# Performance work log

Measured on AMD Instinct MI355X. Metric: run time of the kernel, lower is better.

The kernel has to match this reference:

```python
import jax, jax.numpy as jnp
import numpy as np

EPS = 1e-8
TAU = 1.0


def _spatial_adjacency(segments, n_seg):
    # segments: (B, H, W) int. Counts 4-neighbour pixel adjacencies between segments;
    # diagonal counts pixels per segment (self loops kept).
    B, H, W = segments.shape
    b = jnp.arange(B)[:, None]
    adj = jnp.zeros((B, n_seg, n_seg), jnp.float32)
    flat = segments.reshape(B, -1)
    adj = adj.at[b, flat, flat].add(1.0)  # self loops = segment sizes
    s1 = segments[:, :, :-1].reshape(B, -1)
    s2 = segments[:, :, 1:].reshape(B, -1)
    adj = adj.at[b, s1, s2].add(1.0).at[b, s2, s1].add(1.0)
    v1 = segments[:, :-1, :].reshape(B, -1)
    v2 = segments[:, 1:, :].reshape(B, -1)
    adj = adj.at[b, v1, v2].add(1.0).at[b, v2, v1].add(1.0)
    return adj


def _proximity_adjacency(segments, n_seg):
    adj = _spatial_adjacency(segments, n_seg)
    # zero connections of node 0 except its diagonal
    adj = adj.at[:, 1:, 0].set(0.0).at[:, 0, 1:].set(0.0)
    size_node = jnp.diagonal(adj, axis1=-2, axis2=-1)
    new_diag = adj.sum(axis=2) - size_node + 1.0
    idx = jnp.arange(n_seg)
    adj = adj.at[:, idx, idx].set(new_diag)
    # normalize_adjacency(binarize=True, normalize=False)
    return (adj > 0).astype(jnp.float32)


def setup_inputs() -> dict:
    key = jax.random.key(0)
    k1, k2, k3 = jax.random.split(key, 3)
    B, N, D, R = 8, 2048, 384, 64
    H = W = 256
    x = jax.random.normal(k1, (B, N, D), jnp.float32)
    segments = jax.random.randint(k2, (B, H, W), 0, N, jnp.int64)
    prototypes = jax.random.normal(k3, (1, R, D), jnp.float32)
    return {"x": x, "segments": segments, "prototypes": prototypes}


def reference(x, segments, prototypes):
    B, N, D = x.shape
    prox_adj = _proximity_adjacency(segments, N)  # (B, N, N) binary

    # node-presence mask (B, N)
    b = jnp.arange(B)[:, None]
    flat = segments.reshape(B, -1)
    mask = jnp.zeros((B, N), jnp.float32).at[b, flat].max(1.0)

    # cosine prototype clustering (Q = V = K = Identity)
    protos = prototypes[0]  # (R, D)
    qn = x / jnp.maximum(jnp.linalg.norm(x, axis=-1, keepdims=True), EPS)
    kn = protos / jnp.maximum(jnp.linalg.norm(protos, axis=-1, keepdims=True), EPS)
    Csim = (jnp.einsum('bnd,rd->bnr', qn, kn) + 1.0) * 0.5
    S = Csim / Csim.sum(axis=-1, keepdims=True)  # soft assignment (B, N, R)

    # cluster alignment loss (DEC-style sharpened-target KL, masked over present nodes)
    P = S ** 2 / (S.sum(axis=1, keepdims=True) + EPS)
    P = P / (P.sum(axis=-1, keepdims=True) + EPS)
    kl = (P * (jnp.log(P + EPS) - jnp.log(S + EPS))).sum(axis=-1)  # (B, N)
    loss = (kl * mask).sum() / (mask.sum() + EPS)

    # affinity adjacency from assignments
    C = jax.nn.softmax(S * TAU, axis=-1)  # (B, N, R)
    cn = jnp.linalg.norm(C, axis=-1)  # (B, N)
    proto_adj = jnp.einsum('bnr,bmr->bnm', C, C) / (cn[:, :, None] * cn[:, None, :] + EPS)
    adj = prox_adj * proto_adj
    # normalize_adjacency(normalize=True): row normalization
    adj = adj / (adj.sum(axis=-1, keepdims=True) + EPS)

    out = jnp.einsum('bnm,bmd->bnd', adj, x)  # adj @ values
    return out, segments, loss, C
```

## Files before the change

kernel.cpp:

```cpp
#include <hip/hip_runtime.h>
#include <hip/hip_bf16.h>

#define NB 8
#define NN 2048
#define ND 384
#define NR 64
#define OUT_ELEMS (NB*NN*ND)
#define SEG_ELEMS (NB*256*256)
#define NBLK_LOSS (NB*NN/4)

typedef float  f32x4  __attribute__((ext_vector_type(4)));
typedef short  bf16x8 __attribute__((ext_vector_type(8)));

__device__ inline float wsum(float v){
  #pragma unroll
  for(int o=32;o;o>>=1) v += __shfl_xor(v,o,64);
  return v;
}
__device__ inline float wmax(float v){
  #pragma unroll
  for(int o=32;o;o>>=1) v = fmaxf(v,__shfl_xor(v,o,64));
  return v;
}
__device__ inline unsigned short f2bf(float f){
  unsigned u = __float_as_uint(f);
  return (unsigned short)((u + 0x8000u) >> 16);
}

__device__ __forceinline__ void gl2lds16(const unsigned short* g, unsigned short* s){
  __builtin_amdgcn_global_load_lds(
      (const __attribute__((address_space(1))) unsigned int*)g,
      (__attribute__((address_space(3))) unsigned int*)s,
      16, 0, 0);
}

__global__ void k_proto(const float* __restrict__ protos, float* __restrict__ kn){
  int r = blockIdx.x, l = threadIdx.x;
  float v[6]; float ss = 0.f;
  #pragma unroll
  for(int i=0;i<6;i++){ v[i] = protos[r*ND + l*6 + i]; ss += v[i]*v[i]; }
  ss = wsum(ss);
  float inv = 1.f / fmaxf(sqrtf(ss), 1e-8f);
  #pragma unroll
  for(int i=0;i<6;i++) kn[r*ND + l*6 + i] = v[i]*inv;
}

__global__ __launch_bounds__(1024) void k_seg(const int* __restrict__ seg,
                                              float* __restrict__ mask,
                                              unsigned* __restrict__ prox){
  __shared__ unsigned lm[64*64];
  int tid = threadIdx.x;
  int b  = blockIdx.x & 7;
  int rg = blockIdx.x >> 3;
  int base = rg << 6;
  for(int i=tid; i<64*64; i+=1024) lm[i] = 0u;
  __syncthreads();
  const int* sb = seg + b*65536;

#define PAIR(S, S2) { \
    if((S) != (S2) && (S) != 0 && (S2) != 0){ \
      if(((S )>>6)==rg) atomicOr(&lm[(((S )&63)<<6) + ((S2)>>5)], 1u<<((S2)&31)); \
      if(((S2)>>6)==rg) atomicOr(&lm[(((S2)&63)<<6) + ((S )>>5)], 1u<<((S )&31)); \
    } }

  #pragma unroll 1
  for(int it=0; it<16; ++it){
    int g = it*1024 + tid;
    int p = g*4;
    int i = g >> 6;
    int j = (g & 63)*4;
    int4 a = *(const int4*)(sb + p);
    if((a.x>>6)==rg) mask[(b<<11) + a.x] = 1.f;
    if((a.y>>6)==rg) mask[(b<<11) + a.y] = 1.f;
    if((a.z>>6)==rg) mask[(b<<11) + a.z] = 1.f;
    if((a.w>>6)==rg) mask[(b<<11) + a.w] = 1.f;
    PAIR(a.x, a.y); PAIR(a.y, a.z); PAIR(a.z, a.w);
    if(j < 252){
      int n = sb[p + 4];
      PAIR(a.w, n);
    }
    if(i < 255){
      int4 v = *(const int4*)(sb + p + 256);
      PAIR(a.x, v.x); PAIR(a.y, v.y); PAIR(a.z, v.z); PAIR(a.w, v.w);
    }
  }
#undef PAIR
  __syncthreads();
  unsigned* dst = prox + ((size_t)(b<<11) + base)*64;
  *(uint4*)(dst + tid*4) = *(const uint4*)&lm[tid*4];
}

__global__ __launch_bounds__(256) void k_csim(const float* __restrict__ x,
                                              const float* __restrict__ kn,
                                              float* __restrict__ Sout,
                                              unsigned short* __restrict__ xTbf,
                                              float* __restrict__ part){
  __shared__ float xT[32*68];
  __shared__ float kT[32*68];
  __shared__ float xinvS[64];
  __shared__ float csh[16*64];
  int t = threadIdx.x;
  int m0 = blockIdx.x * 64;
  float acc[4][4] = {};
  int mload = t>>2, koff = (t&3)*8;
  int mb = (t>>4)*4, rb = (t&15)*4;
  float ssq = 0.f;
  for(int c=0;c<12;c++){
    int k0 = c*32;
    __syncthreads();
    const float4* xg = (const float4*)(x + (size_t)(m0+mload)*ND + k0 + koff);
    float4 a = xg[0], bq = xg[1];
    ssq += a.x*a.x + a.y*a.y + a.z*a.z + a.w*a.w
         + bq.x*bq.x + bq.y*bq.y + bq.z*bq.z + bq.w*bq.w;
    xT[(koff+0)*68+mload]=a.x;  xT[(koff+1)*68+mload]=a.y;  xT[(koff+2)*68+mload]=a.z;  xT[(koff+3)*68+mload]=a.w;
    xT[(koff+4)*68+mload]=bq.x; xT[(koff+5)*68+mload]=bq.y; xT[(koff+6)*68+mload]=bq.z; xT[(koff+7)*68+mload]=bq.w;
    const float4* kg = (const float4*)(kn + mload*ND + k0 + koff);
    float4 ka = kg[0], kb = kg[1];
    kT[(koff+0)*68+mload]=ka.x; kT[(koff+1)*68+mload]=ka.y; kT[(koff+2)*68+mload]=ka.z; kT[(koff+3)*68+mload]=ka.w;
    kT[(koff+4)*68+mload]=kb.x; kT[(koff+5)*68+mload]=kb.y; kT[(koff+6)*68+mload]=kb.z; kT[(koff+7)*68+mload]=kb.w;
    __syncthreads();
    {
      int k2 = t>>3, mo = (t&7)*8;
      const float* src = &xT[k2*68 + mo];
      float4 aa = *(const float4*)src;
      float4 bb = *(const float4*)(src+4);
      uint4 o;
      o.x = (unsigned)f2bf(aa.x) | ((unsigned)f2bf(aa.y)<<16);
      o.y = (unsigned)f2bf(aa.z) | ((unsigned)f2bf(aa.w)<<16);
      o.z = (unsigned)f2bf(bb.x) | ((unsigned)f2bf(bb.y)<<16);
      o.w = (unsigned)f2bf(bb.z) | ((unsigned)f2bf(bb.w)<<16);
      int bb2 = m0 >> 11, ml = m0 & 2047;
      *(uint4*)(xTbf + ((size_t)(bb2*ND + k0 + k2))*NN + ml + mo) = o;
    }
    for(int k=0;k<32;k++){
      float xv[4], kv[4];
      *(float4*)xv = *(const float4*)&xT[k*68+mb];
      *(float4*)kv = *(const float4*)&kT[k*68+rb];
      #pragma unroll
      for(int mi=0;mi<4;mi++)
        #pragma unroll
        for(int ri=0;ri<4;ri++) acc[mi][ri] += xv[mi]*kv[ri];
    }
  }
  ssq += __shfl_xor(ssq,1,64);
  ssq += __shfl_xor(ssq,2,64);
  if((t&3)==0) xinvS[mload] = 1.f / fmaxf(sqrtf(ssq), 1e-8f);
  __syncthreads();
  float sv[4][4];
  #pragma unroll
  for(int mi=0;mi<4;mi++){
    float xin = xinvS[mb+mi];
    float rsum = 0.f;
    #pragma unroll
    for(int ri=0;ri<4;ri++){
      float vv = (acc[mi][ri]*xin + 1.f)*0.5f;
      sv[mi][ri] = vv; rsum += vv;
    }
    rsum += __shfl_xor(rsum,1,64);
    rsum += __shfl_xor(rsum,2,64);
    rsum += __shfl_xor(rsum,4,64);
    rsum += __shfl_xor(rsum,8,64);
    float inv = 1.f/rsum;
    #pragma unroll
    for(int ri=0;ri<4;ri++) sv[mi][ri] *= inv;
    *(float4*)&Sout[(size_t)(m0+mb+mi)*NR + rb] = *(const float4*)sv[mi];
  }
  {
    float4 pc;
    pc.x = sv[0][0]+sv[1][0]+sv[2][0]+sv[3][0];
    pc.y = sv[0][1]+sv[1][1]+sv[2][1]+sv[3][1];
    pc.z = sv[0][2]+sv[1][2]+sv[2][2]+sv[3][2];
    pc.w = sv[0][3]+sv[1][3]+sv[2][3]+sv[3][3];
    *(float4*)&csh[(t>>4)*64 + rb] = pc;
  }
  __syncthreads();
  if(t < 64){
    float a = 0.f;
    #pragma unroll
    for(int g=0;g<16;g++) a += csh[g*64 + t];
    part[(size_t)blockIdx.x*64 + t] = a;
  }
}

__global__ void k_lossfc(float* Smat, const float* __restrict__ part,
                         const float* __restrict__ mask,
                         float* __restrict__ klp, float* __restrict__ mp,
                         unsigned short* __restrict__ Kbf){
  __shared__ float shk[4], shm[4];
  int w = threadIdx.x>>6, l = threadIdx.x&63;
  int node = blockIdx.x*4 + w;
  int b = node >> 11;
  float s = Smat[(size_t)node*NR + l];
  float csm = 0.f;
  #pragma unroll
  for(int c=0;c<32;c++) csm += part[(size_t)((b<<5)+c)*64 + l];
  float p = s*s/(csm + 1e-8f);
  float ps = wsum(p);
  float P = p/(ps + 1e-8f);
  float term = P*(logf(P + 1e-8f) - logf(s + 1e-8f));
  float kl = wsum(term);
  if(l==0){ float mv = mask[node]; shk[w] = kl*mv; shm[w] = mv; }
  float mx = wmax(s);
  float e = expf(s - mx);
  float Z = wsum(e);
  float c = e / Z;
  float cn2 = wsum(c*c);
  Smat[(size_t)node*NR + l] = c;
  Kbf[(size_t)node*NR + l] = f2bf(c * rsqrtf(cn2));
  __syncthreads();
  if(threadIdx.x==0){
    klp[blockIdx.x] = shk[0]+shk[1]+shk[2]+shk[3];
    mp [blockIdx.x] = shm[0]+shm[1]+shm[2]+shm[3];
  }
}

__global__ __launch_bounds__(256) void k_qk(const unsigned short* __restrict__ Kbf,
                                            const unsigned* __restrict__ prox,
                                            unsigned short* __restrict__ Pbf){
  __shared__ short Plds[4][16*72];
  int tid = threadIdx.x;
  int w = tid>>6, l = tid&63, q = l>>4, li = l&15;
  int b  = blockIdx.x & 7;
  int qt = (blockIdx.x>>3) & 31;
  int kc = blockIdx.x >> 8;
  const unsigned short* Kb = Kbf + (size_t)b*NN*NR;
  short* myP = Plds[w];

  int arow = qt*64 + w*16 + li;
  bf16x8 af0 = *(const bf16x8*)(Kb + (size_t)arow*NR + q*8);
  bf16x8 af1 = *(const bf16x8*)(Kb + (size_t)arow*NR + 32 + q*8);

  int srow = l>>2, sg = l&3;

  #pragma unroll 1
  for(int kt = kc*4; kt < kc*4 + 4; ++kt){
    uint2 mw[4];
    #pragma unroll
    for(int r=0;r<4;r++)
      mw[r] = *(const uint2*)(prox + ((size_t)(b*NN + qt*64 + w*16 + q*4 + r))*64 + kt*2);
    bf16x8 b0[4], b1[4];
    #pragma unroll
    for(int f=0;f<4;f++){
      const unsigned short* p = Kb + (size_t)(kt*64 + f*16 + li)*NR + q*8;
      b0[f] = *(const bf16x8*)p;
      b1[f] = *(const bf16x8*)(p + 32);
    }
    f32x4 pacc[4] = {(f32x4)(0.f),(f32x4)(0.f),(f32x4)(0.f),(f32x4)(0.f)};
    #pragma unroll
    for(int f=0;f<4;f++){
      pacc[f] = __builtin_amdgcn_mfma_f32_16x16x32_bf16(af0, b0[f], pacc[f], 0,0,0);
      pacc[f] = __builtin_amdgcn_mfma_f32_16x16x32_bf16(af1, b1[f], pacc[f], 0,0,0);
    }
    #pragma unroll
    for(int r=0;r<4;r++){
      int lrow = q*4 + r;
      int brow = w*16 + lrow;
      uint2 m = mw[r];
      if(qt==kt){
        if((brow>>5)==0) m.x |= 1u<<(brow&31); else m.y |= 1u<<(brow&31);
      }
      #pragma unroll
      for(int f=0;f<4;f++){
        unsigned wd = (f<2) ? m.x : m.y;
        float v = ((wd >> ((f&1)*16 + li)) & 1u) ? pacc[f][r] : 0.f;
        myP[lrow*72 + f*16 + li] = (short)f2bf(v);
      }
    }
    const uint4* src = (const uint4*)&myP[srow*72 + sg*16];
    unsigned short* dst = Pbf + ((size_t)(b*NN + qt*64 + w*16 + srow))*NN + kt*64 + sg*16;
    uint4 v0 = src[0], v1 = *(const uint4*)((const short*)src + 8);
    *(uint4*)dst = v0;
    *(uint4*)(dst + 8) = v1;
  }
}

__global__ __launch_bounds__(256, 3) void k_pv(const unsigned short* __restrict__ Pbf,
                                               const unsigned short* __restrict__ xTbf,
                                               float* __restrict__ out){
  __shared__ unsigned short Al[64*64];
  __shared__ unsigned short Bl[128*64];
  int tid = threadIdx.x;
  int w = tid>>6, l = tid&63, q = l>>4, li = l&15;
  int b  = blockIdx.x & 7;
  int mt = (blockIdx.x>>3) & 31;
  int ct = blockIdx.x >> 8;
  int m0 = mt*64;
  int d0 = ct*128;
  const unsigned short* Pb  = Pbf  + (size_t)b*NN*NN;
  const unsigned short* xTb = xTbf + (size_t)b*ND*NN;

  int wr = w & 1, wc = w >> 1;

  int lrow8 = l>>3;
  int sgel  = ((l&7) ^ lrow8) * 8;
  const unsigned short* gsrc[6];
  unsigned short* ldst[6];
  #pragma unroll
  for(int j=0;j<6;j++){
    int id = w*6 + j;
    if(id < 8){
      ldst[j] = Al + id*512;
      gsrc[j] = Pb + (size_t)(m0 + id*8 + lrow8)*NN + sgel;
    }else{
      ldst[j] = Bl + (id-8)*512;
      gsrc[j] = xTb + (size_t)(d0 + (id-8)*8 + lrow8)*NN + sgel;
    }
  }

  f32x4 acc[2][4];
  #pragma unroll
  for(int nc=0;nc<2;nc++)
    #pragma unroll
    for(int t=0;t<4;t++) acc[nc][t] = (f32x4)(0.f);
  f32x4 rs[2] = {(f32x4)(0.f),(f32x4)(0.f)};
  bf16x8 ones;
  #pragma unroll
  for(int i=0;i<8;i++) ones[i] = (short)0x3F80;

  int r7 = li & 7;
  for(int k0=0; k0<NN; k0+=64){
    __syncthreads();
    #pragma unroll
    for(int j=0;j<6;j++) gl2lds16(gsrc[j] + k0, ldst[j]);
    __syncthreads();
    #pragma unroll
    for(int s=0;s<2;s++){
      int ps = ((s*4 + q) ^ r7) * 8;
      bf16x8 a0 = *(const bf16x8*)&Al[(wr*32 +      li)*64 + ps];
      bf16x8 a1 = *(const bf16x8*)&Al[(wr*32 + 16 + li)*64 + ps];
      bf16x8 bv[4];
      #pragma unroll
      for(int t=0;t<4;t++)
        bv[t] = *(const bf16x8*)&Bl[(wc*64 + t*16 + li)*64 + ps];
      #pragma unroll
      for(int t=0;t<4;t++){
        acc[0][t] = __builtin_amdgcn_mfma_f32_16x16x32_bf16(a0, bv[t], acc[0][t], 0,0,0);
        acc[1][t] = __builtin_amdgcn_mfma_f32_16x16x32_bf16(a1, bv[t], acc[1][t], 0,0,0);
      }
      rs[0] = __builtin_amdgcn_mfma_f32_16x16x32_bf16(a0, ones, rs[0], 0,0,0);
      rs[1] = __builtin_amdgcn_mfma_f32_16x16x32_bf16(a1, ones, rs[1], 0,0,0);
    }
  }

  #pragma unroll
  for(int nc=0;nc<2;nc++)
    #pragma unroll
    for(int r=0;r<4;r++){
      int row = m0 + wr*32 + nc*16 + q*4 + r;
      float inv = 1.f/(rs[nc][r] + 1e-8f);
      float* orow = out + ((size_t)(b*NN + row))*ND + d0 + wc*64;
      #pragma unroll
      for(int t=0;t<4;t++)
        orow[t*16 + li] = acc[nc][t][r] * inv;
    }
}

__global__ void k_segout(const int* __restrict__ seg, float* __restrict__ o,
                         const float* __restrict__ klp, const float* __restrict__ mp,
                         float* __restrict__ outLoss){
  int tid = threadIdx.x;
  int i = blockIdx.x*256 + tid;
  o[i] = (float)seg[i];
  if(blockIdx.x==0){
    __shared__ float sa[4], sm[4];
    float a=0.f, m=0.f;
    for(int k=tid; k<NBLK_LOSS; k+=256){ a += klp[k]; m += mp[k]; }
    a = wsum(a); m = wsum(m);
    if((tid&63)==0){ sa[tid>>6]=a; sm[tid>>6]=m; }
    __syncthreads();
    if(tid==0)
      outLoss[0] = (sa[0]+sa[1]+sa[2]+sa[3])/((sm[0]+sm[1]+sm[2]+sm[3])+1e-8f);
  }
}

extern "C" void kernel_launch(void* const* d_in, const int* in_sizes, int n_in,
                              void* d_out, int out_size, void* d_ws, size_t ws_size,
                              hipStream_t stream) {
  const float* x      = (const float*)d_in[0];
  const int*   seg    = (const int*)d_in[1];
  const float* protos = (const float*)d_in[2];

  float* out     = (float*)d_out;
  float* outSeg  = out + OUT_ELEMS;
  float* outLoss = outSeg + SEG_ELEMS;
  float* outC    = outLoss + 1;

  unsigned short* xTbf = (unsigned short*)d_ws;
  unsigned short* Kbf  = xTbf + (size_t)NB*ND*NN;
  unsigned short* Pbf  = Kbf + (size_t)NB*NN*NR;
  float* kn      = (float*)(Pbf + (size_t)NB*NN*NN);
  float* maskp   = kn + NR*ND;
  unsigned* prox = (unsigned*)(maskp + NB*NN);
  float* part    = (float*)(prox + (size_t)NB*NN*64);
  float* klp     = part + NB*32*64;
  float* mp      = klp + NBLK_LOSS;

  hipMemsetAsync(maskp, 0, (size_t)NB*NN*4, stream);

  k_proto <<<dim3(NR),           dim3(64),   0, stream>>>(protos, kn);
  k_seg   <<<dim3(256),          dim3(1024), 0, stream>>>(seg, maskp, prox);
  k_csim  <<<dim3(NB*NN/64),     dim3(256),  0, stream>>>(x, kn, outC, xTbf, part);
  k_lossfc<<<dim3(NBLK_LOSS),    dim3(256),  0, stream>>>(outC, part, maskp, klp, mp, Kbf);
  k_qk    <<<dim3(2048),         dim3(256),  0, stream>>>(Kbf, prox, Pbf);
  k_pv    <<<dim3(768),          dim3(256),  0, stream>>>(Pbf, xTbf, out);
  k_segout<<<dim3(SEG_ELEMS/256),dim3(256),  0, stream>>>(seg, outSeg, klp, mp, outLoss);
}
```

Baseline: 216.5 us.

## Fuse masked affinity QK into PV kernel, dropping the materialized P matrix

Merges the kernel that computed the masked bf16 affinity matrix P into the P@x kernel. Each k-tile of P is now computed with MFMA from the normalized assignment vectors, masked by the proximity bitmap, and written straight into the LDS A-tile. This removes the write and re-read of the 8x2048x2048 bf16 P buffer in global memory plus one launch. In exchange each of the three column-tile blocks recomputes the same QK tile, and the LDS-staging loop now does extra MFMA and masking work before each barrier.

```diff
diff --git a/kernel.cpp b/kernel.cpp
--- a/kernel.cpp
+++ b/kernel.cpp
@@ -214,69 +214,10 @@
   }
 }
 
-__global__ __launch_bounds__(256) void k_qk(const unsigned short* __restrict__ Kbf,
-                                            const unsigned* __restrict__ prox,
-                                            unsigned short* __restrict__ Pbf){
-  __shared__ short Plds[4][16*72];
-  int tid = threadIdx.x;
-  int w = tid>>6, l = tid&63, q = l>>4, li = l&15;
-  int b  = blockIdx.x & 7;
-  int qt = (blockIdx.x>>3) & 31;
-  int kc = blockIdx.x >> 8;
-  const unsigned short* Kb = Kbf + (size_t)b*NN*NR;
-  short* myP = Plds[w];
-
-  int arow = qt*64 + w*16 + li;
-  bf16x8 af0 = *(const bf16x8*)(Kb + (size_t)arow*NR + q*8);
-  bf16x8 af1 = *(const bf16x8*)(Kb + (size_t)arow*NR + 32 + q*8);
-
-  int srow = l>>2, sg = l&3;
-
-  #pragma unroll 1
-  for(int kt = kc*4; kt < kc*4 + 4; ++kt){
-    uint2 mw[4];
-    #pragma unroll
-    for(int r=0;r<4;r++)
-      mw[r] = *(const uint2*)(prox + ((size_t)(b*NN + qt*64 + w*16 + q*4 + r))*64 + kt*2);
-    bf16x8 b0[4], b1[4];
-    #pragma unroll
-    for(int f=0;f<4;f++){
-      const unsigned short* p = Kb + (size_t)(kt*64 + f*16 + li)*NR + q*8;
-      b0[f] = *(const bf16x8*)p;
-      b1[f] = *(const bf16x8*)(p + 32);
-    }
-    f32x4 pacc[4] = {(f32x4)(0.f),(f32x4)(0.f),(f32x4)(0.f),(f32x4)(0.f)};
-    #pragma unroll
-    for(int f=0;f<4;f++){
-      pacc[f] = __builtin_amdgcn_mfma_f32_16x16x32_bf16(af0, b0[f], pacc[f], 0,0,0);
-      pacc[f] = __builtin_amdgcn_mfma_f32_16x16x32_bf16(af1, b1[f], pacc[f], 0,0,0);
-    }
-    #pragma unroll
-    for(int r=0;r<4;r++){
-      int lrow = q*4 + r;
-      int brow = w*16 + lrow;
-      uint2 m = mw[r];
-      if(qt==kt){
-        if((brow>>5)==0) m.x |= 1u<<(brow&31); else m.y |= 1u<<(brow&31);
-      }
-      #pragma unroll
-      for(int f=0;f<4;f++){
-        unsigned wd = (f<2) ? m.x : m.y;
-        float v = ((wd >> ((f&1)*16 + li)) & 1u) ? pacc[f][r] : 0.f;
-        myP[lrow*72 + f*16 + li] = (short)f2bf(v);
-      }
-    }
-    const uint4* src = (const uint4*)&myP[srow*72 + sg*16];
-    unsigned short* dst = Pbf + ((size_t)(b*NN + qt*64 + w*16 + srow))*NN + kt*64 + sg*16;
-    uint4 v0 = src[0], v1 = *(const uint4*)((const short*)src + 8);
-    *(uint4*)dst = v0;
-    *(uint4*)(dst + 8) = v1;
-  }
-}
-
-__global__ __launch_bounds__(256, 3) void k_pv(const unsigned short* __restrict__ Pbf,
-                                               const unsigned short* __restrict__ xTbf,
-                                               float* __restrict__ out){
+__global__ __launch_bounds__(256, 3) void k_qkpv(const unsigned short* __restrict__ Kbf,
+                                                 const unsigned* __restrict__ prox,
+                                                 const unsigned short* __restrict__ xTbf,
+                                                 float* __restrict__ out){
   __shared__ unsigned short Al[64*64];
   __shared__ unsigned short Bl[128*64];
   int tid = threadIdx.x;
@@ -286,26 +227,27 @@
   int ct = blockIdx.x >> 8;
   int m0 = mt*64;
   int d0 = ct*128;
-  const unsigned short* Pb  = Pbf  + (size_t)b*NN*NN;
-  const unsigned short* xTb = xTbf + (size_t)b*ND*NN;
+  const unsigned short* Kb   = Kbf  + (size_t)b*NN*NR;
+  const unsigned short* xTb  = xTbf + (size_t)b*ND*NN;
 
   int wr = w & 1, wc = w >> 1;
 
   int lrow8 = l>>3;
   int sgel  = ((l&7) ^ lrow8) * 8;
-  const unsigned short* gsrc[6];
-  unsigned short* ldst[6];
-  #pragma unroll
-  for(int j=0;j<6;j++){
-    int id = w*6 + j;
-    if(id < 8){
-      ldst[j] = Al + id*512;
-      gsrc[j] = Pb + (size_t)(m0 + id*8 + lrow8)*NN + sgel;
-    }else{
-      ldst[j] = Bl + (id-8)*512;
-      gsrc[j] = xTb + (size_t)(d0 + (id-8)*8 + lrow8)*NN + sgel;
-    }
-  }
+  const unsigned short* gsrc[4];
+  unsigned short* ldst[4];
+  #pragma unroll
+  for(int j=0;j<4;j++){
+    int id = w*4 + j;
+    ldst[j] = Bl + id*512;
+    gsrc[j] = xTb + (size_t)(d0 + id*8 + lrow8)*NN + sgel;
+  }
+
+  const unsigned short* bmp = Kb + (size_t)(m0 + w*16 + li)*NR + q*8;
+  bf16x8 bm0 = *(const bf16x8*)bmp;
+  bf16x8 bm1 = *(const bf16x8*)(bmp + 32);
+  const unsigned* prxp = prox + ((size_t)(b*NN + m0 + w*16 + li))*64;
+  int diagidx = w*16 + li;
 
   f32x4 acc[2][4];
   #pragma unroll
@@ -320,9 +262,43 @@
   int r7 = li & 7;
   for(int k0=0; k0<NN; k0+=64){
     __syncthreads();
-    #pragma unroll
-    for(int j=0;j<6;j++) gl2lds16(gsrc[j] + k0, ldst[j]);
-    __syncthreads();
+    bf16x8 ka0[4], ka1[4];
+    #pragma unroll
+    for(int f=0;f<4;f++){
+      const unsigned short* p = Kb + (size_t)(k0 + f*16 + li)*NR + q*8;
+      ka0[f] = *(const bf16x8*)p;
+      ka1[f] = *(const bf16x8*)(p + 32);
+    }
+    #pragma unroll
+    for(int j=0;j<4;j++) gl2lds16(gsrc[j] + k0, ldst[j]);
+    uint2 mw = *(const uint2*)(prxp + (k0>>5));
+
+    f32x4 pacc[4] = {(f32x4)(0.f),(f32x4)(0.f),(f32x4)(0.f),(f32x4)(0.f)};
+    #pragma unroll
+    for(int f=0;f<4;f++){
+      pacc[f] = __builtin_amdgcn_mfma_f32_16x16x32_bf16(ka0[f], bm0, pacc[f], 0,0,0);
+      pacc[f] = __builtin_amdgcn_mfma_f32_16x16x32_bf16(ka1[f], bm1, pacc[f], 0,0,0);
+    }
+    bool dg = (k0 == m0);
+    #pragma unroll
+    for(int f=0;f<4;f++){
+      unsigned wd = (f<2) ? mw.x : mw.y;
+      float v[4];
+      #pragma unroll
+      for(int r=0;r<4;r++){
+        int bit = ((f&1)*16) + q*4 + r;
+        bool on = (wd >> bit) & 1u;
+        if(dg && (f*16 + q*4 + r) == diagidx) on = true;
+        v[r] = on ? pacc[f][r] : 0.f;
+      }
+      uint2 pk;
+      pk.x = (unsigned)f2bf(v[0]) | ((unsigned)f2bf(v[1])<<16);
+      pk.y = (unsigned)f2bf(v[2]) | ((unsigned)f2bf(v[3])<<16);
+      int eoff = (w*16 + li)*64 + (((f*2 + (q>>1)) ^ r7) * 8) + (q&1)*4;
+      *(uint2*)&Al[eoff] = pk;
+    }
+    __syncthreads();
+
     #pragma unroll
     for(int s=0;s<2;s++){
       int ps = ((s*4 + q) ^ r7) * 8;
@@ -401,7 +377,6 @@
   k_seg   <<<dim3(256),          dim3(1024), 0, stream>>>(seg, maskp, prox);
   k_csim  <<<dim3(NB*NN/64),     dim3(256),  0, stream>>>(x, kn, outC, xTbf, part);
   k_lossfc<<<dim3(NBLK_LOSS),    dim3(256),  0, stream>>>(outC, part, maskp, klp, mp, Kbf);
-  k_qk    <<<dim3(2048),         dim3(256),  0, stream>>>(Kbf, prox, Pbf);
-  k_pv    <<<dim3(768),          dim3(256),  0, stream>>>(Pbf, xTbf, out);
+  k_qkpv  <<<dim3(768),          dim3(256),  0, stream>>>(Kbf, prox, xTbf, out);
   k_segout<<<dim3(SEG_ELEMS/256),dim3(256),  0, stream>>>(seg, outSeg, klp, mp, outLoss);
 }
```

New measurement: 250.3 us. 15.6% more time.
